# Optimization experiments

Measured on AMD Instinct MI355X. Metric: run time of the kernel, lower is better.

The kernel has to match this reference:

```python
import jax, jax.numpy as jnp
import numpy as np

ALPHA = 3.0   # self.alpha
TAU = 0.1     # contrastive temperature
K = 8         # configs.k (top-k hyperedges per node)


def _scale(x, w, ehy, enod):
    """One scale of incidence_matrix_learn.
    x: [B, L, D] series tokens; w: [ws, D] word tokens;
    ehy: [H, D] hyperedge embedding table; enod: [N, D] node embedding table, N = L + ws.
    Returns (binary incidence matrix [N, H] float32, scalar contrastive loss).
    """
    B = x.shape[0]
    # concat_all[i]: cat(x.permute(0,2,1), word_expanded) -> [B, D, N]
    we = jnp.broadcast_to(w.T[None], (B,) + w.T.shape)          # [B, D, ws]
    concat = jnp.concatenate([jnp.transpose(x, (0, 2, 1)), we], axis=-1)  # [B, D, N]
    N, H = enod.shape[0], ehy.shape[0]
    # adjacency: softmax(relu(alpha * nodeec @ hyperen.T)) along hyperedge dim
    a = enod @ ehy.T                                            # [N, H]
    adj = jax.nn.softmax(jax.nn.relu(ALPHA * a), axis=-1)
    # top-k mask + threshold > 0.5 -> binary incidence matrix
    k = min(H, K)
    _, idx = jax.lax.top_k(adj, k)                              # [N, k]
    mask = jnp.zeros_like(adj).at[jnp.arange(N)[:, None], idx].set(1.0)
    adj_bin = ((adj * mask) > 0.5).astype(jnp.float32)          # [N, H]
    # positives: nodes sharing any hyperedge (build_pos_indices_from_edge_index),
    # equivalent to (A A^T > 0) with self excluded; dropping all-zero columns is a no-op here
    P = (adj_bin @ adj_bin.T > 0) & ~jnp.eye(N, dtype=bool)     # [N, N]
    cnt = P.sum(axis=1)                                         # positives per node
    # acl_loss_batched, vectorized over batch and nodes
    nodes = jnp.transpose(concat, (0, 2, 1))                    # [B, N, D]
    nrm = nodes / jnp.maximum(jnp.linalg.norm(nodes, axis=-1, keepdims=True), 1e-12)
    sim = jnp.einsum('bnd,bmd->bnm', nrm, nrm) / TAU            # [B, N, N]
    denom = jax.nn.logsumexp(sim, axis=-1)                      # [B, N]
    pos_mean = jnp.einsum('bnm,nm->bn', sim, P.astype(sim.dtype)) / jnp.maximum(cnt, 1)
    valid = cnt > 0                                             # [N]
    loss_sum = jnp.sum(jnp.where(valid[None, :], denom - pos_mean, 0.0))
    vc = B * valid.sum()
    loss = jnp.where(vc > 0, loss_sum / jnp.maximum(vc, 1), 0.0)
    return adj_bin, loss


def setup_inputs() -> dict:
    key = jax.random.key(0)
    ks = jax.random.split(key, 8)
    B, D = 64, 512
    return dict(
        x0=jax.random.normal(ks[0], (B, 512, D), dtype=jnp.float32),
        x1=jax.random.normal(ks[1], (B, 256, D), dtype=jnp.float32),
        word0=jax.random.normal(ks[2], (128, D), dtype=jnp.float32),
        word1=jax.random.normal(ks[3], (128, D), dtype=jnp.float32),
        embhy0=jax.random.normal(ks[4], (128, D), dtype=jnp.float32),
        embhy1=jax.random.normal(ks[5], (64, D), dtype=jnp.float32),
        embnod0=jax.random.normal(ks[6], (640, D), dtype=jnp.float32),
        embnod1=jax.random.normal(ks[7], (384, D), dtype=jnp.float32),
    )


def reference(x0, x1, word0, word1, embhy0, embhy1, embnod0, embnod1):
    a0, l0 = _scale(x0, word0, embhy0, embnod0)
    a1, l1 = _scale(x1, word1, embhy1, embnod1)
    return (a0, a1, l0 + l1)
```

## Files before the change

### kernel.cpp

```cpp
#include <hip/hip_runtime.h>


#define DDIM 512
#define BATCH 64

typedef __attribute__((ext_vector_type(8))) short short8;
typedef __attribute__((ext_vector_type(4))) float f32x4;

__device__ __forceinline__ unsigned short f2bf(float f) {
  unsigned int u = __float_as_uint(f);
  u += 0x7fffu + ((u >> 16) & 1u);
  return (unsigned short)(u >> 16);
}

__device__ __forceinline__ void async16(const void* g, void* l) {
  __builtin_amdgcn_global_load_lds(
      (const __attribute__((address_space(1))) unsigned int*)g,
      (__attribute__((address_space(3))) unsigned int*)l, 16, 0, 0);
}

__global__ __launch_bounds__(256) void prep_kernel(
    const float* __restrict__ enod0, const float* __restrict__ ehy0,
    const float* __restrict__ enod1, const float* __restrict__ ehy1,
    float* __restrict__ adj0, float* __restrict__ adj1,
    int* __restrict__ labels0, int* __restrict__ labels1,
    const float* __restrict__ x0, const float* __restrict__ w0,
    const float* __restrict__ x1, const float* __restrict__ w1,
    unsigned short* __restrict__ nhat0, unsigned short* __restrict__ nhat1,
    float* __restrict__ acc) {
  const int t = threadIdx.x;
  if (blockIdx.x < 1024) {
    if (blockIdx.x == 0 && t == 0) { acc[0] = 0.f; acc[1] = 0.f; }
    const bool s0 = blockIdx.x < 640;
    const int n = s0 ? blockIdx.x : blockIdx.x - 640;
    const int H = s0 ? 128 : 64;
    const float* enod = s0 ? enod0 : enod1;
    const float* ehy = s0 ? ehy0 : ehy1;
    float* out_adj = s0 ? adj0 : adj1;
    int* labels = s0 ? labels0 : labels1;
    __shared__ float erow[DDIM];
    __shared__ float red[128];
    __shared__ int lab;
    if (t < 128) ((float4*)erow)[t] = ((const float4*)(enod + (size_t)n * DDIM))[t];
    if (t == 0) lab = -1;
    __syncthreads();
    float v = 0.f;
    if (t < H) {
      const float4* hr = (const float4*)(ehy + (size_t)t * DDIM);
      float a = 0.f;
      #pragma unroll 8
      for (int d = 0; d < DDIM / 4; ++d) {
        float4 h = hr[d];
        float4 e = ((const float4*)erow)[d];
        a = fmaf(h.x, e.x, a); a = fmaf(h.y, e.y, a);
        a = fmaf(h.z, e.z, a); a = fmaf(h.w, e.w, a);
      }
      v = fmaxf(0.f, 3.0f * a);
    }
    if (t < 128) red[t] = v;
    __syncthreads();
    for (int s = 64; s > 0; s >>= 1) {
      if (t < s) red[t] = fmaxf(red[t], red[t + s]);
      __syncthreads();
    }
    const float mx = red[0];
    __syncthreads();
    const float e = (t < H) ? __expf(v - mx) : 0.f;
    if (t < 128) red[t] = e;
    __syncthreads();
    for (int s = 64; s > 0; s >>= 1) {
      if (t < s) red[t] += red[t + s];
      __syncthreads();
    }
    const float sum = red[0];
    if (t < H) {
      const float adj = e / sum;
      const float bin = (adj > 0.5f) ? 1.0f : 0.0f;
      out_adj[(size_t)n * H + t] = bin;
      if (bin > 0.f) lab = t;
    }
    __syncthreads();
    if (t == 0) labels[n] = lab;
  } else {
    const int wave = t >> 6;
    const int lane = t & 63;
    const int g = (blockIdx.x - 1024) * 4 + wave;
    const bool s0 = g < BATCH * 640;
    const int gg = s0 ? g : g - BATCH * 640;
    const int N = s0 ? 640 : 384;
    const int L = s0 ? 512 : 256;
    const float* x = s0 ? x0 : x1;
    const float* w = s0 ? w0 : w1;
    unsigned short* nhat = s0 ? nhat0 : nhat1;
    const int b = gg / N;
    const int n = gg - b * N;
    const float* src = (n < L) ? (x + ((size_t)b * L + n) * DDIM)
                               : (w + (size_t)(n - L) * DDIM);
    const float4* rowp = (const float4*)src;
    const float4 v0 = rowp[lane];
    const float4 v1 = rowp[lane + 64];
    float ss = v0.x * v0.x + v0.y * v0.y + v0.z * v0.z + v0.w * v0.w +
               v1.x * v1.x + v1.y * v1.y + v1.z * v1.z + v1.w * v1.w;
    #pragma unroll
    for (int off = 32; off > 0; off >>= 1) ss += __shfl_xor(ss, off);
    const float rinv = 1.0f / fmaxf(sqrtf(ss), 1e-12f);
    ushort4 o0, o1;
    o0.x = f2bf(v0.x * rinv); o0.y = f2bf(v0.y * rinv);
    o0.z = f2bf(v0.z * rinv); o0.w = f2bf(v0.w * rinv);
    o1.x = f2bf(v1.x * rinv); o1.y = f2bf(v1.y * rinv);
    o1.z = f2bf(v1.z * rinv); o1.w = f2bf(v1.w * rinv);
    ushort4* op = (ushort4*)(nhat + ((size_t)b * N + n) * DDIM);
    op[lane] = o0;
    op[lane + 64] = o1;
  }
}

__global__ __launch_bounds__(256) void cnt_kernel(
    const int* __restrict__ labels0, int* __restrict__ cnt0,
    const int* __restrict__ labels1, int* __restrict__ cnt1,
    int* __restrict__ valid) {
  const bool s0 = blockIdx.x == 0;
  const int* labels = s0 ? labels0 : labels1;
  int* cnt = s0 ? cnt0 : cnt1;
  int* validcnt = s0 ? valid : valid + 1;
  const int N = s0 ? 640 : 384;
  __shared__ int lab[640];
  __shared__ int hist[128];
  __shared__ int vc;
  const int t = threadIdx.x;
  if (t == 0) vc = 0;
  if (t < 128) hist[t] = 0;
  for (int i = t; i < N; i += 256) lab[i] = labels[i];
  __syncthreads();
  for (int i = t; i < N; i += 256)
    if (lab[i] >= 0) atomicAdd(&hist[lab[i]], 1);
  __syncthreads();
  int lv = 0;
  for (int i = t; i < N; i += 256) {
    const int c = (lab[i] >= 0) ? hist[lab[i]] - 1 : 0;
    cnt[i] = c;
    if (c > 0) ++lv;
  }
  if (lv > 0) atomicAdd(&vc, lv);
  __syncthreads();
  if (t == 0) *validcnt = vc;
}

__global__ __launch_bounds__(128, 2) void lse_kernel(
    const unsigned short* __restrict__ nhat0, const int* __restrict__ labels0,
    const int* __restrict__ cnt0, const unsigned short* __restrict__ nhat1,
    const int* __restrict__ labels1, const int* __restrict__ cnt1,
    float* __restrict__ loss_acc) {
  __shared__ short8 Bbuf[4][512];
  __shared__ int labS[640];
  __shared__ float redS[64];
  __shared__ float redP[64];
  const int tid = threadIdx.x;
  const bool s0 = blockIdx.x < 640;
  const int i = s0 ? blockIdx.x : blockIdx.x - 640;
  const int N = s0 ? 640 : 384;
  const int ntiles = s0 ? 10 : 6;
  const unsigned short* nhat = s0 ? nhat0 : nhat1;
  const int* labels = s0 ? labels0 : labels1;
  const int* cnt = s0 ? cnt0 : cnt1;
  float* acc_out = s0 ? loss_acc : loss_acc + 1;
  const int b = i & 63;
  const int tn = i >> 6;
  const int n0 = tn * 64;
  const int wave = tid >> 6;
  const int lane = tid & 63;
  const int lrow = lane & 15;
  const int lq = lane >> 4;
  for (int t = tid; t < N; t += 128) labS[t] = labels[t];

  const size_t base = (size_t)b * N * DDIM;
  const int rw0 = n0 + wave * 32;
  const unsigned short* Ap0 = nhat + base + (size_t)(rw0 + lrow) * DDIM + lq * 8;
  const unsigned short* Ap1 = nhat + base + (size_t)(rw0 + 16 + lrow) * DDIM + lq * 8;
  short8 a0[16], a1[16];
  #pragma unroll
  for (int ks = 0; ks < 16; ++ks) {
    a0[ks] = *(const short8*)(Ap0 + ks * 32);
    a1[ks] = *(const short8*)(Ap1 + ks * 32);
  }

  __syncthreads();

  int labn[2][4];
  #pragma unroll
  for (int s = 0; s < 2; ++s)
    #pragma unroll
    for (int r = 0; r < 4; ++r) labn[s][r] = labS[rw0 + s * 16 + lq * 4 + r];

  #pragma unroll
  for (int pc = 0; pc < 3; ++pc) {
    #pragma unroll
    for (int fi = 0; fi < 4; ++fi) {
      const int f = wave * 4 + fi;
      const int j = f >> 1, ks = f & 1;
      const unsigned short* g = nhat + base +
          (size_t)(j * 16 + lrow) * DDIM + pc * 64 + ks * 32 + lq * 8;
      async16(g, &Bbuf[pc][f * 64]);
    }
  }

  float se[2][4] = {{0.f, 0.f, 0.f, 0.f}, {0.f, 0.f, 0.f, 0.f}};
  float pos[2][4] = {{0.f, 0.f, 0.f, 0.f}, {0.f, 0.f, 0.f, 0.f}};

  for (int mt = 0; mt < ntiles; ++mt) {
    const bool last_mt = (mt == ntiles - 1);
    f32x4 acc[4][2];
    #pragma unroll
    for (int j = 0; j < 4; ++j) {
      acc[j][0] = (f32x4){0.f, 0.f, 0.f, 0.f};
      acc[j][1] = (f32x4){0.f, 0.f, 0.f, 0.f};
    }
    #pragma unroll
    for (int kc = 0; kc < 8; ++kc) {
      if (!last_mt || kc < 6) {
        asm volatile("s_waitcnt vmcnt(8)" ::: "memory");
      } else if (kc == 6) {
        asm volatile("s_waitcnt vmcnt(4)" ::: "memory");
      } else {
        asm volatile("s_waitcnt vmcnt(0)" ::: "memory");
      }
      __builtin_amdgcn_s_barrier();
      if (!last_mt || kc < 5) {
        const int mt2 = mt + ((kc + 3) >> 3);
        const int kc2 = (kc + 3) & 7;
        short8* dst = &Bbuf[(kc + 3) & 3][0];
        #pragma unroll
        for (int fi = 0; fi < 4; ++fi) {
          const int f = wave * 4 + fi;
          const int j = f >> 1, ks = f & 1;
          const unsigned short* g = nhat + base +
              (size_t)(mt2 * 64 + j * 16 + lrow) * DDIM +
              kc2 * 64 + ks * 32 + lq * 8;
          async16(g, dst + f * 64);
        }
      }
      const short8* bb = &Bbuf[kc & 3][0];
      #pragma unroll
      for (int ks = 0; ks < 2; ++ks) {
        const short8 b0 = bb[(0 + ks) * 64 + lane];
        const short8 b1 = bb[(2 + ks) * 64 + lane];
        const short8 b2 = bb[(4 + ks) * 64 + lane];
        const short8 b3 = bb[(6 + ks) * 64 + lane];
        const short8 av0 = a0[kc * 2 + ks];
        const short8 av1 = a1[kc * 2 + ks];
        acc[0][0] = __builtin_amdgcn_mfma_f32_16x16x32_bf16(av0, b0, acc[0][0], 0, 0, 0);
        acc[0][1] = __builtin_amdgcn_mfma_f32_16x16x32_bf16(av1, b0, acc[0][1], 0, 0, 0);
        acc[1][0] = __builtin_amdgcn_mfma_f32_16x16x32_bf16(av0, b1, acc[1][0], 0, 0, 0);
        acc[1][1] = __builtin_amdgcn_mfma_f32_16x16x32_bf16(av1, b1, acc[1][1], 0, 0, 0);
        acc[2][0] = __builtin_amdgcn_mfma_f32_16x16x32_bf16(av0, b2, acc[2][0], 0, 0, 0);
        acc[2][1] = __builtin_amdgcn_mfma_f32_16x16x32_bf16(av1, b2, acc[2][1], 0, 0, 0);
        acc[3][0] = __builtin_amdgcn_mfma_f32_16x16x32_bf16(av0, b3, acc[3][0], 0, 0, 0);
        acc[3][1] = __builtin_amdgcn_mfma_f32_16x16x32_bf16(av1, b3, acc[3][1], 0, 0, 0);
      }
    }
    const int m0 = mt * 64;
    #pragma unroll
    for (int j = 0; j < 4; ++j) {
      const int m = m0 + j * 16 + lrow;
      const int labm = labS[m];
      #pragma unroll
      for (int s = 0; s < 2; ++s) {
        const int row0 = rw0 + s * 16 + lq * 4;
        #pragma unroll
        for (int r = 0; r < 4; ++r) {
          const float sim = acc[j][s][r] * 10.0f;
          se[s][r] += __expf(sim - 10.0f);
          if (labn[s][r] >= 0 && labm == labn[s][r] && m != row0 + r)
            pos[s][r] += sim;
        }
      }
    }
  }

  #pragma unroll
  for (int off = 1; off <= 8; off <<= 1) {
    #pragma unroll
    for (int s = 0; s < 2; ++s)
      #pragma unroll
      for (int r = 0; r < 4; ++r) {
        se[s][r] += __shfl_xor(se[s][r], off);
        pos[s][r] += __shfl_xor(pos[s][r], off);
      }
  }
  if (lrow == 0) {
    #pragma unroll
    for (int s = 0; s < 2; ++s)
      #pragma unroll
      for (int r = 0; r < 4; ++r) {
        redS[wave * 32 + s * 16 + lq * 4 + r] = se[s][r];
        redP[wave * 32 + s * 16 + lq * 4 + r] = pos[s][r];
      }
  }
  __syncthreads();
  if (tid < 64) {
    const int c = cnt[n0 + tid];
    if (c > 0)
      atomicAdd(acc_out, (10.0f + logf(redS[tid])) - redP[tid] / (float)c);
  }
}

__global__ void final_kernel(const float* __restrict__ acc,
                             const int* __restrict__ valid,
                             float* __restrict__ out) {
  float l = 0.f;
  if (valid[0] > 0) l += acc[0] / (float)(BATCH * valid[0]);
  if (valid[1] > 0) l += acc[1] / (float)(BATCH * valid[1]);
  out[0] = l;
}

extern "C" void kernel_launch(void* const* d_in, const int* in_sizes, int n_in,
                              void* d_out, int out_size, void* d_ws,
                              size_t ws_size, hipStream_t stream) {
  const float* x0 = (const float*)d_in[0];
  const float* x1 = (const float*)d_in[1];
  const float* w0 = (const float*)d_in[2];
  const float* w1 = (const float*)d_in[3];
  const float* ehy0 = (const float*)d_in[4];
  const float* ehy1 = (const float*)d_in[5];
  const float* enod0 = (const float*)d_in[6];
  const float* enod1 = (const float*)d_in[7];

  float* out = (float*)d_out;
  float* adj0 = out;
  float* adj1 = out + 640 * 128;
  float* lossp = out + 640 * 128 + 384 * 64;

  unsigned short* nhat0 = (unsigned short*)d_ws;
  unsigned short* nhat1 = nhat0 + (size_t)BATCH * 640 * DDIM;
  int* ip = (int*)(nhat1 + (size_t)BATCH * 384 * DDIM);
  int* labels0 = ip;
  int* labels1 = labels0 + 640;
  int* cnt0 = labels1 + 384;
  int* cnt1 = cnt0 + 640;
  int* valid = cnt1 + 384;
  float* acc = (float*)(valid + 2);

  prep_kernel<<<1024 + 16384, 256, 0, stream>>>(
      enod0, ehy0, enod1, ehy1, adj0, adj1, labels0, labels1,
      x0, w0, x1, w1, nhat0, nhat1, acc);
  cnt_kernel<<<2, 256, 0, stream>>>(labels0, cnt0, labels1, cnt1, valid);
  lse_kernel<<<1024, 128, 0, stream>>>(nhat0, labels0, cnt0, nhat1, labels1,
                                       cnt1, acc);
  final_kernel<<<1, 1, 0, stream>>>(acc, valid, lossp);
}
```

Before: 246.8 us.

## Exploit Gram symmetry: compute upper-triangular tiles and reduce partials separately

The LSE kernel now launches one block per upper-triangular 64x64 tile pair per batch instead of one block per row tile that loops over all column tiles. Off-diagonal tiles feed both the row and column statistics, which removes roughly half of the MFMA work. Per-slot partial sums of exp and positive similarity go to a workspace, and a new loss_reduce kernel combines them and applies log and count normalisation. The cost is an extra kernel launch, extra global traffic for the partials, and less per-block pipelining depth because each block now handles only one tile.

```diff
diff --git a/kernel.cpp b/kernel.cpp
--- a/kernel.cpp
+++ b/kernel.cpp
@@ -3,6 +3,7 @@
 
 #define DDIM 512
 #define BATCH 64
+#define NGID 65536
 
 typedef __attribute__((ext_vector_type(8))) short short8;
 typedef __attribute__((ext_vector_type(4))) float f32x4;
@@ -148,132 +149,125 @@
 
 __global__ __launch_bounds__(128, 2) void lse_kernel(
     const unsigned short* __restrict__ nhat0, const int* __restrict__ labels0,
-    const int* __restrict__ cnt0, const unsigned short* __restrict__ nhat1,
-    const int* __restrict__ labels1, const int* __restrict__ cnt1,
-    float* __restrict__ loss_acc) {
-  __shared__ short8 Bbuf[4][512];
-  __shared__ int labS[640];
-  __shared__ float redS[64];
-  __shared__ float redP[64];
+    const unsigned short* __restrict__ nhat1, const int* __restrict__ labels1,
+    float2* __restrict__ sp) {
+  __shared__ short8 Bbuf[3][512];
+  __shared__ float2 redC[2][64];
   const int tid = threadIdx.x;
-  const bool s0 = blockIdx.x < 640;
-  const int i = s0 ? blockIdx.x : blockIdx.x - 640;
+  const bool s0 = blockIdx.x < 3520;
+  const int i = s0 ? blockIdx.x : blockIdx.x - 3520;
+  const int b = i & 63;
+  int p = i >> 6;
+  const int nt = s0 ? 10 : 6;
+  int tu = 0;
+  while (p >= nt - tu) { p -= nt - tu; ++tu; }
+  const int tv = tu + p;
+  const bool diag = (tu == tv);
   const int N = s0 ? 640 : 384;
-  const int ntiles = s0 ? 10 : 6;
   const unsigned short* nhat = s0 ? nhat0 : nhat1;
   const int* labels = s0 ? labels0 : labels1;
-  const int* cnt = s0 ? cnt0 : cnt1;
-  float* acc_out = s0 ? loss_acc : loss_acc + 1;
-  const int b = i & 63;
-  const int tn = i >> 6;
-  const int n0 = tn * 64;
+  const int gbase = s0 ? b * 640 : 40960 + b * 384;
+
   const int wave = tid >> 6;
   const int lane = tid & 63;
   const int lrow = lane & 15;
   const int lq = lane >> 4;
-  for (int t = tid; t < N; t += 128) labS[t] = labels[t];
 
   const size_t base = (size_t)b * N * DDIM;
-  const int rw0 = n0 + wave * 32;
+  const int rw0 = tu * 64 + wave * 32;
   const unsigned short* Ap0 = nhat + base + (size_t)(rw0 + lrow) * DDIM + lq * 8;
-  const unsigned short* Ap1 = nhat + base + (size_t)(rw0 + 16 + lrow) * DDIM + lq * 8;
+  const unsigned short* Ap1 = Ap0 + (size_t)16 * DDIM;
   short8 a0[16], a1[16];
   #pragma unroll
   for (int ks = 0; ks < 16; ++ks) {
     a0[ks] = *(const short8*)(Ap0 + ks * 32);
     a1[ks] = *(const short8*)(Ap1 + ks * 32);
   }
+  int labn[2][4];
+  #pragma unroll
+  for (int s = 0; s < 2; ++s)
+    #pragma unroll
+    for (int r = 0; r < 4; ++r) labn[s][r] = labels[rw0 + s * 16 + lq * 4 + r];
+  int labm[4];
+  #pragma unroll
+  for (int j = 0; j < 4; ++j) labm[j] = labels[tv * 64 + j * 16 + lrow];
 
   __syncthreads();
 
-  int labn[2][4];
-  #pragma unroll
-  for (int s = 0; s < 2; ++s)
-    #pragma unroll
-    for (int r = 0; r < 4; ++r) labn[s][r] = labS[rw0 + s * 16 + lq * 4 + r];
-
-  #pragma unroll
-  for (int pc = 0; pc < 3; ++pc) {
+  const unsigned short* Bp = nhat + base + (size_t)(tv * 64) * DDIM;
+  const int f0 = wave * 4;
+  #pragma unroll
+  for (int pc = 0; pc < 2; ++pc) {
     #pragma unroll
     for (int fi = 0; fi < 4; ++fi) {
-      const int f = wave * 4 + fi;
-      const int j = f >> 1, ks = f & 1;
-      const unsigned short* g = nhat + base +
-          (size_t)(j * 16 + lrow) * DDIM + pc * 64 + ks * 32 + lq * 8;
-      async16(g, &Bbuf[pc][f * 64]);
-    }
-  }
-
-  float se[2][4] = {{0.f, 0.f, 0.f, 0.f}, {0.f, 0.f, 0.f, 0.f}};
-  float pos[2][4] = {{0.f, 0.f, 0.f, 0.f}, {0.f, 0.f, 0.f, 0.f}};
-
-  for (int mt = 0; mt < ntiles; ++mt) {
-    const bool last_mt = (mt == ntiles - 1);
-    f32x4 acc[4][2];
-    #pragma unroll
-    for (int j = 0; j < 4; ++j) {
-      acc[j][0] = (f32x4){0.f, 0.f, 0.f, 0.f};
-      acc[j][1] = (f32x4){0.f, 0.f, 0.f, 0.f};
-    }
-    #pragma unroll
-    for (int kc = 0; kc < 8; ++kc) {
-      if (!last_mt || kc < 6) {
-        asm volatile("s_waitcnt vmcnt(8)" ::: "memory");
-      } else if (kc == 6) {
-        asm volatile("s_waitcnt vmcnt(4)" ::: "memory");
-      } else {
-        asm volatile("s_waitcnt vmcnt(0)" ::: "memory");
-      }
-      __builtin_amdgcn_s_barrier();
-      if (!last_mt || kc < 5) {
-        const int mt2 = mt + ((kc + 3) >> 3);
-        const int kc2 = (kc + 3) & 7;
-        short8* dst = &Bbuf[(kc + 3) & 3][0];
-        #pragma unroll
-        for (int fi = 0; fi < 4; ++fi) {
-          const int f = wave * 4 + fi;
-          const int j = f >> 1, ks = f & 1;
-          const unsigned short* g = nhat + base +
-              (size_t)(mt2 * 64 + j * 16 + lrow) * DDIM +
-              kc2 * 64 + ks * 32 + lq * 8;
-          async16(g, dst + f * 64);
+      const int f = f0 + fi, j = f >> 1, ks = f & 1;
+      async16(Bp + (size_t)(j * 16 + lrow) * DDIM + pc * 64 + ks * 32 + lq * 8,
+              &Bbuf[pc][f * 64]);
+    }
+  }
+
+  f32x4 acc[4][2];
+  #pragma unroll
+  for (int j = 0; j < 4; ++j) {
+    acc[j][0] = (f32x4){0.f, 0.f, 0.f, 0.f};
+    acc[j][1] = (f32x4){0.f, 0.f, 0.f, 0.f};
+  }
+  #pragma unroll
+  for (int kc = 0; kc < 8; ++kc) {
+    if (kc < 7) asm volatile("s_waitcnt vmcnt(4)" ::: "memory");
+    else        asm volatile("s_waitcnt vmcnt(0)" ::: "memory");
+    __builtin_amdgcn_s_barrier();
+    if (kc < 6) {
+      short8* dst = &Bbuf[(kc + 2) % 3][0];
+      #pragma unroll
+      for (int fi = 0; fi < 4; ++fi) {
+        const int f = f0 + fi, j = f >> 1, ks = f & 1;
+        async16(Bp + (size_t)(j * 16 + lrow) * DDIM + (kc + 2) * 64 + ks * 32 + lq * 8,
+                dst + f * 64);
+      }
+    }
+    const short8* bb = &Bbuf[kc % 3][0];
+    #pragma unroll
+    for (int ks = 0; ks < 2; ++ks) {
+      const short8 b0 = bb[(0 + ks) * 64 + lane];
+      const short8 b1 = bb[(2 + ks) * 64 + lane];
+      const short8 b2 = bb[(4 + ks) * 64 + lane];
+      const short8 b3 = bb[(6 + ks) * 64 + lane];
+      const short8 av0 = a0[kc * 2 + ks];
+      const short8 av1 = a1[kc * 2 + ks];
+      acc[0][0] = __builtin_amdgcn_mfma_f32_16x16x32_bf16(av0, b0, acc[0][0], 0, 0, 0);
+      acc[0][1] = __builtin_amdgcn_mfma_f32_16x16x32_bf16(av1, b0, acc[0][1], 0, 0, 0);
+      acc[1][0] = __builtin_amdgcn_mfma_f32_16x16x32_bf16(av0, b1, acc[1][0], 0, 0, 0);
+      acc[1][1] = __builtin_amdgcn_mfma_f32_16x16x32_bf16(av1, b1, acc[1][1], 0, 0, 0);
+      acc[2][0] = __builtin_amdgcn_mfma_f32_16x16x32_bf16(av0, b2, acc[2][0], 0, 0, 0);
+      acc[2][1] = __builtin_amdgcn_mfma_f32_16x16x32_bf16(av1, b2, acc[2][1], 0, 0, 0);
+      acc[3][0] = __builtin_amdgcn_mfma_f32_16x16x32_bf16(av0, b3, acc[3][0], 0, 0, 0);
+      acc[3][1] = __builtin_amdgcn_mfma_f32_16x16x32_bf16(av1, b3, acc[3][1], 0, 0, 0);
+    }
+  }
+
+  float rSE[2][4] = {{0.f, 0.f, 0.f, 0.f}, {0.f, 0.f, 0.f, 0.f}};
+  float rPOS[2][4] = {{0.f, 0.f, 0.f, 0.f}, {0.f, 0.f, 0.f, 0.f}};
+  float cSE[4] = {0.f, 0.f, 0.f, 0.f};
+  float cPOS[4] = {0.f, 0.f, 0.f, 0.f};
+  #pragma unroll
+  for (int j = 0; j < 4; ++j) {
+    const int v = tv * 64 + j * 16 + lrow;
+    #pragma unroll
+    for (int s = 0; s < 2; ++s) {
+      const int u0 = rw0 + s * 16 + lq * 4;
+      #pragma unroll
+      for (int r = 0; r < 4; ++r) {
+        const float sim = acc[j][s][r] * 10.0f;
+        const float e = __expf(sim - 10.0f);
+        rSE[s][r] += e;
+        const bool match = (labn[s][r] >= 0) && (labm[j] == labn[s][r]);
+        if (match && v != u0 + r) rPOS[s][r] += sim;
+        if (!diag) {
+          cSE[j] += e;
+          if (match) cPOS[j] += sim;
         }
       }
-      const short8* bb = &Bbuf[kc & 3][0];
-      #pragma unroll
-      for (int ks = 0; ks < 2; ++ks) {
-        const short8 b0 = bb[(0 + ks) * 64 + lane];
-        const short8 b1 = bb[(2 + ks) * 64 + lane];
-        const short8 b2 = bb[(4 + ks) * 64 + lane];
-        const short8 b3 = bb[(6 + ks) * 64 + lane];
-        const short8 av0 = a0[kc * 2 + ks];
-        const short8 av1 = a1[kc * 2 + ks];
-        acc[0][0] = __builtin_amdgcn_mfma_f32_16x16x32_bf16(av0, b0, acc[0][0], 0, 0, 0);
-        acc[0][1] = __builtin_amdgcn_mfma_f32_16x16x32_bf16(av1, b0, acc[0][1], 0, 0, 0);
-        acc[1][0] = __builtin_amdgcn_mfma_f32_16x16x32_bf16(av0, b1, acc[1][0], 0, 0, 0);
-        acc[1][1] = __builtin_amdgcn_mfma_f32_16x16x32_bf16(av1, b1, acc[1][1], 0, 0, 0);
-        acc[2][0] = __builtin_amdgcn_mfma_f32_16x16x32_bf16(av0, b2, acc[2][0], 0, 0, 0);
-        acc[2][1] = __builtin_amdgcn_mfma_f32_16x16x32_bf16(av1, b2, acc[2][1], 0, 0, 0);
-        acc[3][0] = __builtin_amdgcn_mfma_f32_16x16x32_bf16(av0, b3, acc[3][0], 0, 0, 0);
-        acc[3][1] = __builtin_amdgcn_mfma_f32_16x16x32_bf16(av1, b3, acc[3][1], 0, 0, 0);
-      }
-    }
-    const int m0 = mt * 64;
-    #pragma unroll
-    for (int j = 0; j < 4; ++j) {
-      const int m = m0 + j * 16 + lrow;
-      const int labm = labS[m];
-      #pragma unroll
-      for (int s = 0; s < 2; ++s) {
-        const int row0 = rw0 + s * 16 + lq * 4;
-        #pragma unroll
-        for (int r = 0; r < 4; ++r) {
-          const float sim = acc[j][s][r] * 10.0f;
-          se[s][r] += __expf(sim - 10.0f);
-          if (labn[s][r] >= 0 && labm == labn[s][r] && m != row0 + r)
-            pos[s][r] += sim;
-        }
-      }
     }
   }
 
@@ -283,8 +277,8 @@
     for (int s = 0; s < 2; ++s)
       #pragma unroll
       for (int r = 0; r < 4; ++r) {
-        se[s][r] += __shfl_xor(se[s][r], off);
-        pos[s][r] += __shfl_xor(pos[s][r], off);
+        rSE[s][r] += __shfl_xor(rSE[s][r], off);
+        rPOS[s][r] += __shfl_xor(rPOS[s][r], off);
       }
   }
   if (lrow == 0) {
@@ -292,15 +286,70 @@
     for (int s = 0; s < 2; ++s)
       #pragma unroll
       for (int r = 0; r < 4; ++r) {
-        redS[wave * 32 + s * 16 + lq * 4 + r] = se[s][r];
-        redP[wave * 32 + s * 16 + lq * 4 + r] = pos[s][r];
-      }
-  }
+        const int u = rw0 + s * 16 + lq * 4 + r;
+        float2 st; st.x = rSE[s][r]; st.y = rPOS[s][r];
+        sp[(size_t)tv * NGID + gbase + u] = st;
+      }
+  }
+
+  if (!diag) {
+    #pragma unroll
+    for (int off = 16; off <= 32; off <<= 1) {
+      #pragma unroll
+      for (int j = 0; j < 4; ++j) {
+        cSE[j] += __shfl_xor(cSE[j], off);
+        cPOS[j] += __shfl_xor(cPOS[j], off);
+      }
+    }
+    if (lane < 16) {
+      #pragma unroll
+      for (int j = 0; j < 4; ++j) {
+        float2 st; st.x = cSE[j]; st.y = cPOS[j];
+        redC[wave][j * 16 + lane] = st;
+      }
+    }
+    __syncthreads();
+    if (tid < 64) {
+      const float2 c0 = redC[0][tid];
+      const float2 c1 = redC[1][tid];
+      const int v = tv * 64 + tid;
+      float2 st; st.x = c0.x + c1.x; st.y = c0.y + c1.y;
+      sp[(size_t)tu * NGID + gbase + v] = st;
+    }
+  }
+}
+
+__global__ __launch_bounds__(256) void loss_reduce(
+    const float2* __restrict__ sp, const int* __restrict__ cnt0,
+    const int* __restrict__ cnt1, float* __restrict__ acc) {
+  __shared__ float r0[4], r1[4];
+  const int t = threadIdx.x;
+  float l0 = 0.f, l1 = 0.f;
+  for (int g = blockIdx.x * 256 + t; g < NGID; g += 64 * 256) {
+    const bool is0 = g < 40960;
+    const int nslots = is0 ? 10 : 6;
+    float se = 0.f, pos = 0.f;
+    for (int s = 0; s < nslots; ++s) {
+      const float2 v = sp[(size_t)s * NGID + g];
+      se += v.x; pos += v.y;
+    }
+    const int n = is0 ? (g % 640) : ((g - 40960) % 384);
+    const int c = is0 ? cnt0[n] : cnt1[n];
+    if (c > 0) {
+      const float v = (10.0f + logf(se)) - pos / (float)c;
+      if (is0) l0 += v; else l1 += v;
+    }
+  }
+  #pragma unroll
+  for (int off = 32; off > 0; off >>= 1) {
+    l0 += __shfl_xor(l0, off);
+    l1 += __shfl_xor(l1, off);
+  }
+  if ((t & 63) == 0) { r0[t >> 6] = l0; r1[t >> 6] = l1; }
   __syncthreads();
-  if (tid < 64) {
-    const int c = cnt[n0 + tid];
-    if (c > 0)
-      atomicAdd(acc_out, (10.0f + logf(redS[tid])) - redP[tid] / (float)c);
+  if (t == 0) {
+    atomicAdd(&acc[0], r0[0] + r0[1] + r0[2] + r0[3]);
+    atomicAdd(&acc[1], r1[0] + r1[1] + r1[2] + r1[3]);
   }
 }
 
@@ -339,12 +388,13 @@
   int* cnt1 = cnt0 + 640;
   int* valid = cnt1 + 384;
   float* acc = (float*)(valid + 2);
+  float2* sp = (float2*)((((size_t)(acc + 2)) + 255) & ~(size_t)255);
 
   prep_kernel<<<1024 + 16384, 256, 0, stream>>>(
       enod0, ehy0, enod1, ehy1, adj0, adj1, labels0, labels1,
       x0, w0, x1, w1, nhat0, nhat1, acc);
   cnt_kernel<<<2, 256, 0, stream>>>(labels0, cnt0, labels1, cnt1, valid);
-  lse_kernel<<<1024, 128, 0, stream>>>(nhat0, labels0, cnt0, nhat1, labels1,
-                                       cnt1, acc);
+  lse_kernel<<<4864, 128, 0, stream>>>(nhat0, labels0, nhat1, labels1, sp);
+  loss_reduce<<<64, 256, 0, stream>>>(sp, cnt0, cnt1, acc);
   final_kernel<<<1, 1, 0, stream>>>(acc, valid, lossp);
 }
```

Measured after the change: 256.7 us. 1.04x slower.
